# Kernel tuning notes

Hardware: AMD Instinct MI355X
Metric: run time of the kernel (lower is better)

The kernel has to match this reference:

```python
import jax, jax.numpy as jnp
import numpy as np

WINDOW = 3      # neighbor_cand_window / neighbor_ment_window default
RHO = 1.0
THRED = 0.8     # sim_thred default
EPS = 1e-8      # torch cosine_similarity eps
B, C, D = 2048, 16, 256


def setup_inputs() -> dict:
    key = jax.random.key(0)
    k1, k2 = jax.random.split(key)
    cand_emb = jax.random.normal(k1, (B * C, D), dtype=jnp.float32)
    # num_mentions acts as a 0/1 validity mask per (mention, candidate)
    num_mentions = jax.random.randint(k2, (B, C), 0, 2).astype(jnp.int32)
    return {"cand_emb": cand_emb, "num_mentions": num_mentions}


def _shifted_copies(emb, left_mask, right_mask, window, cand_num):
    # Replicates iterated leftNeighbor / rightNeighbor: shift rows by cand_num
    # and re-apply the mask after every shift (cumulative masking).
    zeros = jnp.zeros((cand_num, emb.shape[1]), emb.dtype)
    lefts, cur = [], emb
    for _ in range(window):
        cur = jnp.concatenate([zeros, cur[:-cand_num]], axis=0) * left_mask
        lefts.append(cur)
    rights, cur = [], emb
    for _ in range(window):
        cur = jnp.concatenate([cur[cand_num:], zeros], axis=0) * right_mask
        rights.append(cur)
    return lefts, rights


def _forward(cand_emb, num_mentions):
    batch_size, cand_num = num_mentions.shape
    dim = cand_emb.shape[1]
    right_mask = num_mentions.astype(cand_emb.dtype)                       # [B, C]
    left_mask = jnp.concatenate(
        [jnp.zeros((1, cand_num), cand_emb.dtype), right_mask[:-1]], axis=0)
    lm = left_mask.reshape(-1, 1)    # [B*C, 1], broadcasts over dim
    rm = right_mask.reshape(-1, 1)

    lefts, rights = _shifted_copies(cand_emb, lm, rm, WINDOW, cand_num)

    # getNeighborMentionEmbeddingsForCandidate: mean over 2*window shifted copies
    neigh_emb = jnp.mean(jnp.stack(lefts + rights, axis=0), axis=0)        # [B*C, D]

    # buildGraph: cosine similarity of each candidate against every candidate
    # of each shifted copy, block-structured (no [N, 2W*C, D] materialization).
    cand3 = cand_emb.reshape(batch_size, cand_num, dim)
    nc = jnp.linalg.norm(cand3, axis=-1)                                   # [B, C]
    parts = []
    for s in lefts + rights:
        s3 = s.reshape(batch_size, cand_num, dim)
        ns = jnp.linalg.norm(s3, axis=-1)                                  # [B, C]
        dot = jnp.einsum('bid,bjd->bij', cand3, s3)
        sim = dot / jnp.maximum(nc[:, :, None] * ns[:, None, :], EPS)
        # clamp(sim, thred, 1) then zero everything <= thred
        sim = jnp.where(sim > THRED, jnp.clip(sim, THRED, 1.0), 0.0)
        parts.append(sim)
    adj = jnp.concatenate(parts, axis=2).reshape(batch_size * cand_num, -1)
    ones_col = jnp.ones((batch_size * cand_num, 1), cand_emb.dtype)
    adj = jnp.concatenate([adj * RHO, ones_col], axis=1)
    adj = adj / jnp.maximum(jnp.sum(jnp.abs(adj), axis=1, keepdims=True), 1e-12)

    # [B*C, D + 2*WINDOW*C + 1]
    return jnp.concatenate([neigh_emb, adj], axis=1)


def reference(cand_emb, num_mentions):
    return _forward(cand_emb, num_mentions)
```

## Files before the change

### kernel.cpp

```cpp
#include <hip/hip_runtime.h>

#define NB 2048
#define NC 16
#define ND 256
#define OUTW 353
#define THRED 0.8f

typedef short bf16x8 __attribute__((ext_vector_type(8)));
typedef float f32x4 __attribute__((ext_vector_type(4)));

__device__ __forceinline__ unsigned short f2bf(float x) {
    unsigned int u = __float_as_uint(x);
    u += 0x7FFFu + ((u >> 16) & 1u);
    return (unsigned short)(u >> 16);
}

__device__ __forceinline__ bf16x8 cvt8(const float4& a, const float4& b) {
    bf16x8 r;
    r[0] = (short)f2bf(a.x); r[1] = (short)f2bf(a.y);
    r[2] = (short)f2bf(a.z); r[3] = (short)f2bf(a.w);
    r[4] = (short)f2bf(b.x); r[5] = (short)f2bf(b.y);
    r[6] = (short)f2bf(b.z); r[7] = (short)f2bf(b.w);
    return r;
}

__global__ __launch_bounds__(256, 2) void fused_kernel(const float* __restrict__ e,
                                                       const int* __restrict__ nm,
                                                       float* __restrict__ out) {
    const int bid = blockIdx.x;
    const int sb  = (bid & 7) * 64 + (bid >> 3);
    const int w   = threadIdx.x >> 6;
    const int l   = threadIdx.x & 63;
    const int col = l & 15, hi = l >> 4;
    const int b   = sb * 4 + w;
    const int koff = hi * 8;

    float nmv[6];
#pragma unroll
    for (int u = 0; u < 6; ++u) {
        int gb = b + u - 3;
        nmv[u] = (gb >= 0 && gb < NB) ? (float)nm[gb * NC + col] : 0.f;
    }
    float maskv[6];
    maskv[0] = nmv[2];
    maskv[1] = nmv[2] * nmv[1];
    maskv[2] = maskv[1] * nmv[0];
    maskv[3] = nmv[3];
    maskv[4] = nmv[3] * nmv[4];
    maskv[5] = maskv[4] * nmv[5];

    const float* rp0 = e + ((size_t)b * NC + col) * ND + koff;
    float4 s[16];
#pragma unroll
    for (int c = 0; c < 8; ++c) {
        s[2 * c]     = *reinterpret_cast<const float4*>(rp0 + c * 32);
        s[2 * c + 1] = *reinterpret_cast<const float4*>(rp0 + c * 32 + 4);
    }
    bf16x8 af[8];
    float ssq = 0.f;
#pragma unroll
    for (int c = 0; c < 8; ++c) {
        const float4 a = s[2 * c], bb = s[2 * c + 1];
        af[c] = cvt8(a, bb);
        ssq = fmaf(a.x, a.x, ssq);  ssq = fmaf(a.y, a.y, ssq);
        ssq = fmaf(a.z, a.z, ssq);  ssq = fmaf(a.w, a.w, ssq);
        ssq = fmaf(bb.x, bb.x, ssq); ssq = fmaf(bb.y, bb.y, ssq);
        ssq = fmaf(bb.z, bb.z, ssq); ssq = fmaf(bb.w, bb.w, ssq);
    }
    ssq += __shfl_xor(ssq, 16, 64);
    ssq += __shfl_xor(ssq, 32, 64);
    const float nrm_own = sqrtf(ssq);

    const int offs[6] = {-1, -2, -3, 1, 2, 3};
    f32x4 acc[6];
    float nbn[6];
    float nacc[64];
#pragma unroll
    for (int q = 0; q < 64; ++q) nacc[q] = 0.f;

#pragma unroll
    for (int p = 0; p < 6; ++p) {
        acc[p] = (f32x4){0.f, 0.f, 0.f, 0.f};
        nbn[p] = 0.f;
        const int gb = b + offs[p];
        if (gb >= 0 && gb < NB) {
            const float* rp = e + ((size_t)gb * NC + col) * ND + koff;
#pragma unroll
            for (int c = 0; c < 8; ++c) {
                s[2 * c]     = *reinterpret_cast<const float4*>(rp + c * 32);
                s[2 * c + 1] = *reinterpret_cast<const float4*>(rp + c * 32 + 4);
            }
            float sq = 0.f;
            const float m = maskv[p];
#pragma unroll
            for (int c = 0; c < 8; ++c) {
                const float4 a = s[2 * c], bb = s[2 * c + 1];
                bf16x8 bf = cvt8(a, bb);
                acc[p] = __builtin_amdgcn_mfma_f32_16x16x32_bf16(af[c], bf, acc[p], 0, 0, 0);
                sq = fmaf(a.x, a.x, sq);  sq = fmaf(a.y, a.y, sq);
                sq = fmaf(a.z, a.z, sq);  sq = fmaf(a.w, a.w, sq);
                sq = fmaf(bb.x, bb.x, sq); sq = fmaf(bb.y, bb.y, sq);
                sq = fmaf(bb.z, bb.z, sq); sq = fmaf(bb.w, bb.w, sq);
                nacc[c * 8 + 0] = fmaf(m, a.x,  nacc[c * 8 + 0]);
                nacc[c * 8 + 1] = fmaf(m, a.y,  nacc[c * 8 + 1]);
                nacc[c * 8 + 2] = fmaf(m, a.z,  nacc[c * 8 + 2]);
                nacc[c * 8 + 3] = fmaf(m, a.w,  nacc[c * 8 + 3]);
                nacc[c * 8 + 4] = fmaf(m, bb.x, nacc[c * 8 + 4]);
                nacc[c * 8 + 5] = fmaf(m, bb.y, nacc[c * 8 + 5]);
                nacc[c * 8 + 6] = fmaf(m, bb.z, nacc[c * 8 + 6]);
                nacc[c * 8 + 7] = fmaf(m, bb.w, nacc[c * 8 + 7]);
            }
            sq += __shfl_xor(sq, 16, 64);
            sq += __shfl_xor(sq, 32, 64);
            nbn[p] = sqrtf(sq);
        }
    }

    float na[4];
#pragma unroll
    for (int r = 0; r < 4; ++r) na[r] = __shfl(nrm_own, hi * 4 + r, 16);

    float sim[6][4];
    float rowsum[4] = {0.f, 0.f, 0.f, 0.f};
#pragma unroll
    for (int p = 0; p < 6; ++p) {
        const bool mv = (maskv[p] != 0.f);
#pragma unroll
        for (int r = 0; r < 4; ++r) {
            float qd = acc[p][r] / fmaxf(na[r] * nbn[p], 1e-8f);
            float sv = (mv && qd > THRED) ? fminf(qd, 1.f) : 0.f;
            sim[p][r] = sv;
            rowsum[r] += sv;
        }
    }
#pragma unroll
    for (int r = 0; r < 4; ++r) {
#pragma unroll
        for (int o = 1; o < 16; o <<= 1) rowsum[r] += __shfl_xor(rowsum[r], o, 16);
    }

#pragma unroll
    for (int r = 0; r < 4; ++r) {
        const float inv = 1.0f / fmaxf(rowsum[r] + 1.0f, 1e-12f);
        float* orow = out + (size_t)(b * NC + hi * 4 + r) * OUTW;
#pragma unroll
        for (int p = 0; p < 6; ++p) orow[ND + p * NC + col] = sim[p][r] * inv;
        if (col == 0) orow[ND + 96] = inv;
    }

    const float s6 = 1.0f / 6.0f;
    float* nrow = out + (size_t)(b * NC + col) * OUTW + koff;
#pragma unroll
    for (int c = 0; c < 8; ++c) {
#pragma unroll
        for (int ee = 0; ee < 8; ++ee)
            nrow[c * 32 + ee] = nacc[c * 8 + ee] * s6;
    }
}

extern "C" void kernel_launch(void* const* d_in, const int* in_sizes, int n_in,
                              void* d_out, int out_size, void* d_ws, size_t ws_size,
                              hipStream_t stream) {
    const float* e = (const float*)d_in[0];
    const int* nmv = (const int*)d_in[1];
    float* out     = (float*)d_out;
    fused_kernel<<<NB / 4, 256, 0, stream>>>(e, nmv, out);
}
```

Before: 41.45 us.

## Split sim and neighbor-mean work into separate blocks with per-side wave split

The single fused kernel is split into two block roles: sim blocks, where each pair of waves covers one mention's left and right neighbor sets and the two halves share row sums through LDS, and neighbor-mean blocks, where each wave computes one output row with coalesced float4 loads and stores and skips masked-out neighbor rows. The grid grows from 512 to 9216 blocks, assigned per XCD, and the 64-register nacc array goes away. This should cut register pressure and strided stores and raise occupancy, at the cost of reading the embeddings a second time in the neighbor-mean blocks and adding a block-level barrier.

```diff
diff --git a/kernel.cpp b/kernel.cpp
--- a/kernel.cpp
+++ b/kernel.cpp
@@ -5,9 +5,14 @@
 #define ND 256
 #define OUTW 353
 #define THRED 0.8f
+#define SIM_PER_XCD 128
+#define NEIGH_PER_XCD 1024
+#define PER_XCD 1152
+#define NBLK 9216
 
 typedef short bf16x8 __attribute__((ext_vector_type(8)));
 typedef float f32x4 __attribute__((ext_vector_type(4)));
+typedef float f32x4a __attribute__((ext_vector_type(4), aligned(4)));
 
 __device__ __forceinline__ unsigned short f2bf(float x) {
     unsigned int u = __float_as_uint(x);
@@ -24,30 +29,69 @@
     return r;
 }
 
-__global__ __launch_bounds__(256, 2) void fused_kernel(const float* __restrict__ e,
-                                                       const int* __restrict__ nm,
-                                                       float* __restrict__ out) {
-    const int bid = blockIdx.x;
-    const int sb  = (bid & 7) * 64 + (bid >> 3);
+__global__ __launch_bounds__(256) void fused_kernel(const float* __restrict__ e,
+                                                    const int* __restrict__ nm,
+                                                    float* __restrict__ out) {
+    __shared__ float lsum[4][16];
+
+    const int xcd = blockIdx.x & 7;
+    const int idx = blockIdx.x >> 3;
     const int w   = threadIdx.x >> 6;
     const int l   = threadIdx.x & 63;
-    const int col = l & 15, hi = l >> 4;
-    const int b   = sb * 4 + w;
+
+    if (idx >= SIM_PER_XCD) {
+        const int nrow = (xcd * NEIGH_PER_XCD + (idx - SIM_PER_XCD)) * 4 + w;
+        const int b = nrow >> 4, c = nrow & 15;
+
+        float a1 = (b - 1 >= 0) ? (float)nm[(b - 1) * NC + c] : 0.f;
+        float a2 = (b - 2 >= 0) ? (float)nm[(b - 2) * NC + c] : 0.f;
+        float a3 = (b - 3 >= 0) ? (float)nm[(b - 3) * NC + c] : 0.f;
+        float r0 = (float)nm[b * NC + c];
+        float r1 = (b + 1 < NB) ? (float)nm[(b + 1) * NC + c] : 0.f;
+        float r2 = (b + 2 < NB) ? (float)nm[(b + 2) * NC + c] : 0.f;
+        float mk[6];
+        mk[0] = a1; mk[1] = a1 * a2; mk[2] = a1 * a2 * a3;
+        mk[3] = r0; mk[4] = r0 * r1; mk[5] = r0 * r1 * r2;
+        const int offs[6] = {-1, -2, -3, 1, 2, 3};
+
+        f32x4 acc = (f32x4){0.f, 0.f, 0.f, 0.f};
+#pragma unroll
+        for (int p = 0; p < 6; ++p) {
+            const int gb = b + offs[p];
+            if (mk[p] != 0.f && gb >= 0 && gb < NB) {
+                const float4 v = *reinterpret_cast<const float4*>(
+                    e + ((size_t)gb * NC + c) * ND + l * 4);
+                acc[0] = fmaf(mk[p], v.x, acc[0]);
+                acc[1] = fmaf(mk[p], v.y, acc[1]);
+                acc[2] = fmaf(mk[p], v.z, acc[2]);
+                acc[3] = fmaf(mk[p], v.w, acc[3]);
+            }
+        }
+        const float s6 = 1.0f / 6.0f;
+        f32x4 r;
+        r[0] = acc[0] * s6; r[1] = acc[1] * s6; r[2] = acc[2] * s6; r[3] = acc[3] * s6;
+        *reinterpret_cast<f32x4a*>(out + (size_t)nrow * OUTW + l * 4) = r;
+        return;
+    }
+
+    const int simpair = xcd * SIM_PER_XCD + idx;
+    const int b    = simpair * 2 + (w >> 1);
+    const int side = w & 1;
+    const int col  = l & 15, hi = l >> 4;
     const int koff = hi * 8;
 
-    float nmv[6];
-#pragma unroll
-    for (int u = 0; u < 6; ++u) {
-        int gb = b + u - 3;
-        nmv[u] = (gb >= 0 && gb < NB) ? (float)nm[gb * NC + col] : 0.f;
+    float mk[3];
+    if (side == 0) {
+        float a1 = (b - 1 >= 0) ? (float)nm[(b - 1) * NC + col] : 0.f;
+        float a2 = (b - 2 >= 0) ? (float)nm[(b - 2) * NC + col] : 0.f;
+        float a3 = (b - 3 >= 0) ? (float)nm[(b - 3) * NC + col] : 0.f;
+        mk[0] = a1; mk[1] = a1 * a2; mk[2] = a1 * a2 * a3;
+    } else {
+        float a0 = (float)nm[b * NC + col];
+        float a1 = (b + 1 < NB) ? (float)nm[(b + 1) * NC + col] : 0.f;
+        float a2 = (b + 2 < NB) ? (float)nm[(b + 2) * NC + col] : 0.f;
+        mk[0] = a0; mk[1] = a0 * a1; mk[2] = a0 * a1 * a2;
     }
-    float maskv[6];
-    maskv[0] = nmv[2];
-    maskv[1] = nmv[2] * nmv[1];
-    maskv[2] = maskv[1] * nmv[0];
-    maskv[3] = nmv[3];
-    maskv[4] = nmv[3] * nmv[4];
-    maskv[5] = maskv[4] * nmv[5];
 
     const float* rp0 = e + ((size_t)b * NC + col) * ND + koff;
     float4 s[16];
@@ -71,18 +115,13 @@
     ssq += __shfl_xor(ssq, 32, 64);
     const float nrm_own = sqrtf(ssq);
 
-    const int offs[6] = {-1, -2, -3, 1, 2, 3};
-    f32x4 acc[6];
-    float nbn[6];
-    float nacc[64];
+    f32x4 acc[3];
+    float nbn[3];
 #pragma unroll
-    for (int q = 0; q < 64; ++q) nacc[q] = 0.f;
-
-#pragma unroll
-    for (int p = 0; p < 6; ++p) {
-        acc[p] = (f32x4){0.f, 0.f, 0.f, 0.f};
-        nbn[p] = 0.f;
-        const int gb = b + offs[p];
+    for (int pp = 0; pp < 3; ++pp) {
+        acc[pp] = (f32x4){0.f, 0.f, 0.f, 0.f};
+        nbn[pp] = 0.f;
+        const int gb = b + (side ? (pp + 1) : -(pp + 1));
         if (gb >= 0 && gb < NB) {
             const float* rp = e + ((size_t)gb * NC + col) * ND + koff;
 #pragma unroll
@@ -91,28 +130,19 @@
                 s[2 * c + 1] = *reinterpret_cast<const float4*>(rp + c * 32 + 4);
             }
             float sq = 0.f;
-            const float m = maskv[p];
 #pragma unroll
             for (int c = 0; c < 8; ++c) {
                 const float4 a = s[2 * c], bb = s[2 * c + 1];
                 bf16x8 bf = cvt8(a, bb);
-                acc[p] = __builtin_amdgcn_mfma_f32_16x16x32_bf16(af[c], bf, acc[p], 0, 0, 0);
+                acc[pp] = __builtin_amdgcn_mfma_f32_16x16x32_bf16(af[c], bf, acc[pp], 0, 0, 0);
                 sq = fmaf(a.x, a.x, sq);  sq = fmaf(a.y, a.y, sq);
                 sq = fmaf(a.z, a.z, sq);  sq = fmaf(a.w, a.w, sq);
                 sq = fmaf(bb.x, bb.x, sq); sq = fmaf(bb.y, bb.y, sq);
                 sq = fmaf(bb.z, bb.z, sq); sq = fmaf(bb.w, bb.w, sq);
-                nacc[c * 8 + 0] = fmaf(m, a.x,  nacc[c * 8 + 0]);
-                nacc[c * 8 + 1] = fmaf(m, a.y,  nacc[c * 8 + 1]);
-                nacc[c * 8 + 2] = fmaf(m, a.z,  nacc[c * 8 + 2]);
-                nacc[c * 8 + 3] = fmaf(m, a.w,  nacc[c * 8 + 3]);
-                nacc[c * 8 + 4] = fmaf(m, bb.x, nacc[c * 8 + 4]);
-                nacc[c * 8 + 5] = fmaf(m, bb.y, nacc[c * 8 + 5]);
-                nacc[c * 8 + 6] = fmaf(m, bb.z, nacc[c * 8 + 6]);
-                nacc[c * 8 + 7] = fmaf(m, bb.w, nacc[c * 8 + 7]);
             }
             sq += __shfl_xor(sq, 16, 64);
             sq += __shfl_xor(sq, 32, 64);
-            nbn[p] = sqrtf(sq);
+            nbn[pp] = sqrtf(sq);
         }
     }
 
@@ -120,16 +150,16 @@
 #pragma unroll
     for (int r = 0; r < 4; ++r) na[r] = __shfl(nrm_own, hi * 4 + r, 16);
 
-    float sim[6][4];
+    float sim[3][4];
     float rowsum[4] = {0.f, 0.f, 0.f, 0.f};
 #pragma unroll
-    for (int p = 0; p < 6; ++p) {
-        const bool mv = (maskv[p] != 0.f);
+    for (int pp = 0; pp < 3; ++pp) {
+        const bool mv = (mk[pp] != 0.f);
 #pragma unroll
         for (int r = 0; r < 4; ++r) {
-            float qd = acc[p][r] / fmaxf(na[r] * nbn[p], 1e-8f);
+            float qd = acc[pp][r] / fmaxf(na[r] * nbn[pp], 1e-8f);
             float sv = (mv && qd > THRED) ? fminf(qd, 1.f) : 0.f;
-            sim[p][r] = sv;
+            sim[pp][r] = sv;
             rowsum[r] += sv;
         }
     }
@@ -139,22 +169,22 @@
         for (int o = 1; o < 16; o <<= 1) rowsum[r] += __shfl_xor(rowsum[r], o, 16);
     }
 
+    if (col == 0) {
+#pragma unroll
+        for (int r = 0; r < 4; ++r) lsum[w][hi * 4 + r] = rowsum[r];
+    }
+    __syncthreads();
+
+    const int p_base = side * 3;
 #pragma unroll
     for (int r = 0; r < 4; ++r) {
-        const float inv = 1.0f / fmaxf(rowsum[r] + 1.0f, 1e-12f);
+        const float tot = rowsum[r] + lsum[w ^ 1][hi * 4 + r];
+        const float inv = 1.0f / fmaxf(tot + 1.0f, 1e-12f);
         float* orow = out + (size_t)(b * NC + hi * 4 + r) * OUTW;
 #pragma unroll
-        for (int p = 0; p < 6; ++p) orow[ND + p * NC + col] = sim[p][r] * inv;
-        if (col == 0) orow[ND + 96] = inv;
-    }
-
-    const float s6 = 1.0f / 6.0f;
-    float* nrow = out + (size_t)(b * NC + col) * OUTW + koff;
-#pragma unroll
-    for (int c = 0; c < 8; ++c) {
-#pragma unroll
-        for (int ee = 0; ee < 8; ++ee)
-            nrow[c * 32 + ee] = nacc[c * 8 + ee] * s6;
+        for (int pp = 0; pp < 3; ++pp)
+            orow[ND + (p_base + pp) * NC + col] = sim[pp][r] * inv;
+        if (side == 0 && col == 0) orow[ND + 96] = inv;
     }
 }
 
@@ -164,5 +194,5 @@
     const float* e = (const float*)d_in[0];
     const int* nmv = (const int*)d_in[1];
     float* out     = (float*)d_out;
-    fused_kernel<<<NB / 4, 256, 0, stream>>>(e, nmv, out);
+    fused_kernel<<<NBLK, 256, 0, stream>>>(e, nmv, out);
 }
```

Result: slower. 57.47 us (+38.6%).

## Split each batch's K dimension across four waves with LDS reduction

Applied to the files above, without the earlier changes.

Each block now handles one batch item instead of four, and its four waves each take a quarter of the 256-wide feature dimension. Per-wave partial dot products and squared norms are reduced through shared memory before wave 0 finishes the similarity and normalization. This cuts register pressure (16 accumulators instead of 64), raises occupancy, and launches four times as many blocks to hide global load latency. It also switches to the native bf16 conversion and vectorized neighbor-mean stores. Boundary neighbors are clamped rather than skipped, with masks zeroing their contributions. In exchange it adds a block barrier, shared-memory traffic, and idle waves during the epilogue.

```diff
diff --git a/kernel.cpp b/kernel.cpp
--- a/kernel.cpp
+++ b/kernel.cpp
@@ -8,126 +8,180 @@
 
 typedef short bf16x8 __attribute__((ext_vector_type(8)));
 typedef float f32x4 __attribute__((ext_vector_type(4)));
-
-__device__ __forceinline__ unsigned short f2bf(float x) {
-    unsigned int u = __float_as_uint(x);
-    u += 0x7FFFu + ((u >> 16) & 1u);
-    return (unsigned short)(u >> 16);
+typedef float f32x4a __attribute__((ext_vector_type(4), aligned(4)));
+
+__device__ __forceinline__ short f2s(float x) {
+    __bf16 h = (__bf16)x;
+    return __builtin_bit_cast(short, h);
 }
 
 __device__ __forceinline__ bf16x8 cvt8(const float4& a, const float4& b) {
     bf16x8 r;
-    r[0] = (short)f2bf(a.x); r[1] = (short)f2bf(a.y);
-    r[2] = (short)f2bf(a.z); r[3] = (short)f2bf(a.w);
-    r[4] = (short)f2bf(b.x); r[5] = (short)f2bf(b.y);
-    r[6] = (short)f2bf(b.z); r[7] = (short)f2bf(b.w);
+    r[0] = f2s(a.x); r[1] = f2s(a.y); r[2] = f2s(a.z); r[3] = f2s(a.w);
+    r[4] = f2s(b.x); r[5] = f2s(b.y); r[6] = f2s(b.z); r[7] = f2s(b.w);
     return r;
 }
 
-__global__ __launch_bounds__(256, 2) void fused_kernel(const float* __restrict__ e,
+__global__ __launch_bounds__(256, 4) void fused_kernel(const float* __restrict__ e,
                                                        const int* __restrict__ nm,
                                                        float* __restrict__ out) {
+    __shared__ float red[4][64][33];
+
     const int bid = blockIdx.x;
-    const int sb  = (bid & 7) * 64 + (bid >> 3);
-    const int w   = threadIdx.x >> 6;
+    const int b   = (bid & 7) * 256 + (bid >> 3);
+    const int q   = threadIdx.x >> 6;
     const int l   = threadIdx.x & 63;
     const int col = l & 15, hi = l >> 4;
-    const int b   = sb * 4 + w;
-    const int koff = hi * 8;
-
-    float nmv[6];
-#pragma unroll
-    for (int u = 0; u < 6; ++u) {
-        int gb = b + u - 3;
-        nmv[u] = (gb >= 0 && gb < NB) ? (float)nm[gb * NC + col] : 0.f;
-    }
-    float maskv[6];
-    maskv[0] = nmv[2];
-    maskv[1] = nmv[2] * nmv[1];
-    maskv[2] = maskv[1] * nmv[0];
-    maskv[3] = nmv[3];
-    maskv[4] = nmv[3] * nmv[4];
-    maskv[5] = maskv[4] * nmv[5];
+    const int koff = q * 64 + hi * 8;
+
+    const int bm1 = (b >= 1) ? b - 1 : 0;
+    const int bm2 = (b >= 2) ? b - 2 : 0;
+    const int bm3 = (b >= 3) ? b - 3 : 0;
+    const int bp1 = (b + 1 < NB) ? b + 1 : NB - 1;
+    const int bp2 = (b + 2 < NB) ? b + 2 : NB - 1;
+    const int bp3 = (b + 3 < NB) ? b + 3 : NB - 1;
+
+    const float a1 = (b >= 1) ? (float)nm[bm1 * NC + col] : 0.f;
+    const float a2 = (b >= 2) ? (float)nm[bm2 * NC + col] : 0.f;
+    const float a3 = (b >= 3) ? (float)nm[bm3 * NC + col] : 0.f;
+    const float r0 = (float)nm[b * NC + col];
+    const float r1 = (b + 1 < NB) ? (float)nm[bp1 * NC + col] : 0.f;
+    const float r2 = (b + 2 < NB) ? (float)nm[bp2 * NC + col] : 0.f;
+
+    float em[6];
+    em[0] = a1;
+    em[1] = a1 * a2;
+    em[2] = a1 * a2 * a3;
+    em[3] = (b + 1 < NB) ? r0 : 0.f;
+    em[4] = (b + 2 < NB) ? r0 * r1 : 0.f;
+    em[5] = (b + 3 < NB) ? r0 * r1 * r2 : 0.f;
+
+    const int gbs[6] = {bm1, bm2, bm3, bp1, bp2, bp3};
 
     const float* rp0 = e + ((size_t)b * NC + col) * ND + koff;
-    float4 s[16];
-#pragma unroll
-    for (int c = 0; c < 8; ++c) {
-        s[2 * c]     = *reinterpret_cast<const float4*>(rp0 + c * 32);
-        s[2 * c + 1] = *reinterpret_cast<const float4*>(rp0 + c * 32 + 4);
-    }
-    bf16x8 af[8];
-    float ssq = 0.f;
-#pragma unroll
-    for (int c = 0; c < 8; ++c) {
-        const float4 a = s[2 * c], bb = s[2 * c + 1];
-        af[c] = cvt8(a, bb);
-        ssq = fmaf(a.x, a.x, ssq);  ssq = fmaf(a.y, a.y, ssq);
-        ssq = fmaf(a.z, a.z, ssq);  ssq = fmaf(a.w, a.w, ssq);
-        ssq = fmaf(bb.x, bb.x, ssq); ssq = fmaf(bb.y, bb.y, ssq);
-        ssq = fmaf(bb.z, bb.z, ssq); ssq = fmaf(bb.w, bb.w, ssq);
-    }
-    ssq += __shfl_xor(ssq, 16, 64);
-    ssq += __shfl_xor(ssq, 32, 64);
-    const float nrm_own = sqrtf(ssq);
-
-    const int offs[6] = {-1, -2, -3, 1, 2, 3};
+    float4 s0 = *reinterpret_cast<const float4*>(rp0);
+    float4 s1 = *reinterpret_cast<const float4*>(rp0 + 4);
+    float4 s2 = *reinterpret_cast<const float4*>(rp0 + 32);
+    float4 s3 = *reinterpret_cast<const float4*>(rp0 + 36);
+    bf16x8 af0 = cvt8(s0, s1);
+    bf16x8 af1 = cvt8(s2, s3);
+
+    float ssqp[7];
+    {
+        float sq = 0.f;
+        sq = fmaf(s0.x, s0.x, sq); sq = fmaf(s0.y, s0.y, sq);
+        sq = fmaf(s0.z, s0.z, sq); sq = fmaf(s0.w, s0.w, sq);
+        sq = fmaf(s1.x, s1.x, sq); sq = fmaf(s1.y, s1.y, sq);
+        sq = fmaf(s1.z, s1.z, sq); sq = fmaf(s1.w, s1.w, sq);
+        sq = fmaf(s2.x, s2.x, sq); sq = fmaf(s2.y, s2.y, sq);
+        sq = fmaf(s2.z, s2.z, sq); sq = fmaf(s2.w, s2.w, sq);
+        sq = fmaf(s3.x, s3.x, sq); sq = fmaf(s3.y, s3.y, sq);
+        sq = fmaf(s3.z, s3.z, sq); sq = fmaf(s3.w, s3.w, sq);
+        ssqp[0] = sq;
+    }
+
     f32x4 acc[6];
-    float nbn[6];
-    float nacc[64];
-#pragma unroll
-    for (int q = 0; q < 64; ++q) nacc[q] = 0.f;
+    float nacc[16];
+#pragma unroll
+    for (int k = 0; k < 16; ++k) nacc[k] = 0.f;
 
 #pragma unroll
     for (int p = 0; p < 6; ++p) {
-        acc[p] = (f32x4){0.f, 0.f, 0.f, 0.f};
-        nbn[p] = 0.f;
-        const int gb = b + offs[p];
-        if (gb >= 0 && gb < NB) {
-            const float* rp = e + ((size_t)gb * NC + col) * ND + koff;
-#pragma unroll
-            for (int c = 0; c < 8; ++c) {
-                s[2 * c]     = *reinterpret_cast<const float4*>(rp + c * 32);
-                s[2 * c + 1] = *reinterpret_cast<const float4*>(rp + c * 32 + 4);
-            }
-            float sq = 0.f;
-            const float m = maskv[p];
-#pragma unroll
-            for (int c = 0; c < 8; ++c) {
-                const float4 a = s[2 * c], bb = s[2 * c + 1];
-                bf16x8 bf = cvt8(a, bb);
-                acc[p] = __builtin_amdgcn_mfma_f32_16x16x32_bf16(af[c], bf, acc[p], 0, 0, 0);
-                sq = fmaf(a.x, a.x, sq);  sq = fmaf(a.y, a.y, sq);
-                sq = fmaf(a.z, a.z, sq);  sq = fmaf(a.w, a.w, sq);
-                sq = fmaf(bb.x, bb.x, sq); sq = fmaf(bb.y, bb.y, sq);
-                sq = fmaf(bb.z, bb.z, sq); sq = fmaf(bb.w, bb.w, sq);
-                nacc[c * 8 + 0] = fmaf(m, a.x,  nacc[c * 8 + 0]);
-                nacc[c * 8 + 1] = fmaf(m, a.y,  nacc[c * 8 + 1]);
-                nacc[c * 8 + 2] = fmaf(m, a.z,  nacc[c * 8 + 2]);
-                nacc[c * 8 + 3] = fmaf(m, a.w,  nacc[c * 8 + 3]);
-                nacc[c * 8 + 4] = fmaf(m, bb.x, nacc[c * 8 + 4]);
-                nacc[c * 8 + 5] = fmaf(m, bb.y, nacc[c * 8 + 5]);
-                nacc[c * 8 + 6] = fmaf(m, bb.z, nacc[c * 8 + 6]);
-                nacc[c * 8 + 7] = fmaf(m, bb.w, nacc[c * 8 + 7]);
-            }
-            sq += __shfl_xor(sq, 16, 64);
-            sq += __shfl_xor(sq, 32, 64);
-            nbn[p] = sqrtf(sq);
+        const float* rp = e + ((size_t)gbs[p] * NC + col) * ND + koff;
+        float4 t0 = *reinterpret_cast<const float4*>(rp);
+        float4 t1 = *reinterpret_cast<const float4*>(rp + 4);
+        float4 t2 = *reinterpret_cast<const float4*>(rp + 32);
+        float4 t3 = *reinterpret_cast<const float4*>(rp + 36);
+        bf16x8 bf0 = cvt8(t0, t1);
+        bf16x8 bf1 = cvt8(t2, t3);
+        f32x4 ac = (f32x4){0.f, 0.f, 0.f, 0.f};
+        ac = __builtin_amdgcn_mfma_f32_16x16x32_bf16(af0, bf0, ac, 0, 0, 0);
+        ac = __builtin_amdgcn_mfma_f32_16x16x32_bf16(af1, bf1, ac, 0, 0, 0);
+        acc[p] = ac;
+
+        float sq = 0.f;
+        sq = fmaf(t0.x, t0.x, sq); sq = fmaf(t0.y, t0.y, sq);
+        sq = fmaf(t0.z, t0.z, sq); sq = fmaf(t0.w, t0.w, sq);
+        sq = fmaf(t1.x, t1.x, sq); sq = fmaf(t1.y, t1.y, sq);
+        sq = fmaf(t1.z, t1.z, sq); sq = fmaf(t1.w, t1.w, sq);
+        sq = fmaf(t2.x, t2.x, sq); sq = fmaf(t2.y, t2.y, sq);
+        sq = fmaf(t2.z, t2.z, sq); sq = fmaf(t2.w, t2.w, sq);
+        sq = fmaf(t3.x, t3.x, sq); sq = fmaf(t3.y, t3.y, sq);
+        sq = fmaf(t3.z, t3.z, sq); sq = fmaf(t3.w, t3.w, sq);
+        ssqp[1 + p] = sq;
+
+        const float m = em[p];
+        nacc[0]  = fmaf(m, t0.x, nacc[0]);  nacc[1]  = fmaf(m, t0.y, nacc[1]);
+        nacc[2]  = fmaf(m, t0.z, nacc[2]);  nacc[3]  = fmaf(m, t0.w, nacc[3]);
+        nacc[4]  = fmaf(m, t1.x, nacc[4]);  nacc[5]  = fmaf(m, t1.y, nacc[5]);
+        nacc[6]  = fmaf(m, t1.z, nacc[6]);  nacc[7]  = fmaf(m, t1.w, nacc[7]);
+        nacc[8]  = fmaf(m, t2.x, nacc[8]);  nacc[9]  = fmaf(m, t2.y, nacc[9]);
+        nacc[10] = fmaf(m, t2.z, nacc[10]); nacc[11] = fmaf(m, t2.w, nacc[11]);
+        nacc[12] = fmaf(m, t3.x, nacc[12]); nacc[13] = fmaf(m, t3.y, nacc[13]);
+        nacc[14] = fmaf(m, t3.z, nacc[14]); nacc[15] = fmaf(m, t3.w, nacc[15]);
+    }
+
+    {
+        const float s6 = 1.0f / 6.0f;
+        float* nrow = out + (size_t)(b * NC + col) * OUTW + koff;
+        f32x4 v;
+        v[0] = nacc[0] * s6;  v[1] = nacc[1] * s6;  v[2] = nacc[2] * s6;  v[3] = nacc[3] * s6;
+        *reinterpret_cast<f32x4a*>(nrow) = v;
+        v[0] = nacc[4] * s6;  v[1] = nacc[5] * s6;  v[2] = nacc[6] * s6;  v[3] = nacc[7] * s6;
+        *reinterpret_cast<f32x4a*>(nrow + 4) = v;
+        v[0] = nacc[8] * s6;  v[1] = nacc[9] * s6;  v[2] = nacc[10] * s6; v[3] = nacc[11] * s6;
+        *reinterpret_cast<f32x4a*>(nrow + 32) = v;
+        v[0] = nacc[12] * s6; v[1] = nacc[13] * s6; v[2] = nacc[14] * s6; v[3] = nacc[15] * s6;
+        *reinterpret_cast<f32x4a*>(nrow + 36) = v;
+    }
+
+    {
+        float* myred = &red[q][l][0];
+#pragma unroll
+        for (int p = 0; p < 6; ++p) {
+#pragma unroll
+            for (int r = 0; r < 4; ++r) myred[p * 4 + r] = acc[p][r];
         }
+#pragma unroll
+        for (int tt = 0; tt < 7; ++tt) myred[24 + tt] = ssqp[tt];
+    }
+    __syncthreads();
+    if (q != 0) return;
+
+#pragma unroll
+    for (int ww = 1; ww < 4; ++ww) {
+        const float* o = &red[ww][l][0];
+#pragma unroll
+        for (int p = 0; p < 6; ++p) {
+#pragma unroll
+            for (int r = 0; r < 4; ++r) acc[p][r] += o[p * 4 + r];
+        }
+#pragma unroll
+        for (int tt = 0; tt < 7; ++tt) ssqp[tt] += o[24 + tt];
+    }
+
+    float norms[7];
+#pragma unroll
+    for (int tt = 0; tt < 7; ++tt) {
+        float v = ssqp[tt];
+        v += __shfl_xor(v, 16, 64);
+        v += __shfl_xor(v, 32, 64);
+        norms[tt] = sqrtf(v);
     }
 
     float na[4];
 #pragma unroll
-    for (int r = 0; r < 4; ++r) na[r] = __shfl(nrm_own, hi * 4 + r, 16);
+    for (int r = 0; r < 4; ++r) na[r] = __shfl(norms[0], hi * 4 + r, 16);
 
     float sim[6][4];
     float rowsum[4] = {0.f, 0.f, 0.f, 0.f};
 #pragma unroll
     for (int p = 0; p < 6; ++p) {
-        const bool mv = (maskv[p] != 0.f);
+        const bool mv = (em[p] != 0.f);
+        const float nbv = norms[1 + p];
 #pragma unroll
         for (int r = 0; r < 4; ++r) {
-            float qd = acc[p][r] / fmaxf(na[r] * nbn[p], 1e-8f);
+            float qd = acc[p][r] / fmaxf(na[r] * nbv, 1e-8f);
             float sv = (mv && qd > THRED) ? fminf(qd, 1.f) : 0.f;
             sim[p][r] = sv;
             rowsum[r] += sv;
@@ -144,17 +198,9 @@
         const float inv = 1.0f / fmaxf(rowsum[r] + 1.0f, 1e-12f);
         float* orow = out + (size_t)(b * NC + hi * 4 + r) * OUTW;
 #pragma unroll
-        for (int p = 0; p < 6; ++p) orow[ND + p * NC + col] = sim[p][r] * inv;
+        for (int p = 0; p < 6; ++p)
+            orow[ND + p * NC + col] = sim[p][r] * inv;
         if (col == 0) orow[ND + 96] = inv;
-    }
-
-    const float s6 = 1.0f / 6.0f;
-    float* nrow = out + (size_t)(b * NC + col) * OUTW + koff;
-#pragma unroll
-    for (int c = 0; c < 8; ++c) {
-#pragma unroll
-        for (int ee = 0; ee < 8; ++ee)
-            nrow[c * 32 + ee] = nacc[c * 8 + ee] * s6;
     }
 }
 
@@ -164,5 +210,5 @@
     const float* e = (const float*)d_in[0];
     const int* nmv = (const int*)d_in[1];
     float* out     = (float*)d_out;
-    fused_kernel<<<NB / 4, 256, 0, stream>>>(e, nmv, out);
-}
+    fused_kernel<<<NB, 256, 0, stream>>>(e, nmv, out);
+}
```

After: 49.94 us. 1.2x slower.
